# Performance work log

Hardware: AMD Instinct MI355X
Metric: run time of the kernel (lower is better)

Reference implementation:

```python
import jax, jax.numpy as jnp
import numpy as np

D_MODEL = 768
N_HEADS = 12
D_FF = 3072
EPS = 1e-5


def _dense_params(key, d_in, d_out):
    kw, kb = jax.random.split(key)
    bound = 1.0 / np.sqrt(d_in)
    W = jax.random.uniform(kw, (d_in, d_out), minval=-bound, maxval=bound, dtype=jnp.float32)
    b = jax.random.uniform(kb, (d_out,), minval=-bound, maxval=bound, dtype=jnp.float32)
    return W, b


def setup_inputs() -> dict:
    key = jax.random.key(0)
    ks = jax.random.split(key, 8)
    x = jax.random.normal(ks[0], (2, 2048, D_MODEL), dtype=jnp.float32)
    wq, bq = _dense_params(ks[1], D_MODEL, D_MODEL)
    wk, bk = _dense_params(ks[2], D_MODEL, D_MODEL)
    wv, bv = _dense_params(ks[3], D_MODEL, D_MODEL)
    wo, bo = _dense_params(ks[4], D_MODEL, D_MODEL)
    w1, b1 = _dense_params(ks[5], D_MODEL, D_FF)
    w2, b2 = _dense_params(ks[6], D_FF, D_MODEL)
    g1 = jnp.ones((D_MODEL,), jnp.float32); be1 = jnp.zeros((D_MODEL,), jnp.float32)
    g2 = jnp.ones((D_MODEL,), jnp.float32); be2 = jnp.zeros((D_MODEL,), jnp.float32)
    return {"x": x, "wq": wq, "bq": bq, "wk": wk, "bk": bk, "wv": wv, "bv": bv,
            "wo": wo, "bo": bo, "w1": w1, "b1": b1, "w2": w2, "b2": b2,
            "g1": g1, "be1": be1, "g2": g2, "be2": be2}


def _layernorm(x, g, b):
    mu = jnp.mean(x, axis=-1, keepdims=True)
    var = jnp.mean(jnp.square(x - mu), axis=-1, keepdims=True)
    return (x - mu) * jax.lax.rsqrt(var + EPS) * g + b


def reference(x, wq, bq, wk, bk, wv, bv, wo, bo, w1, b1, w2, b2, g1, be1, g2, be2):
    B, S, D = x.shape
    H, dk = N_HEADS, D // N_HEADS
    # projections -> [B, H, S, dk]
    def split_heads(t):
        return t.reshape(B, S, H, dk).transpose(0, 2, 1, 3)
    q = split_heads(x @ wq + bq)
    k = split_heads(x @ wk + bk)
    v = split_heads(x @ wv + bv)
    scores = jnp.einsum('bhqd,bhkd->bhqk', q, k) / np.sqrt(dk).astype(np.float32)
    causal = jnp.tril(jnp.ones((S, S), dtype=bool))  # True = keep
    scores = jnp.where(causal, scores, -jnp.inf)
    attn = jax.nn.softmax(scores, axis=-1)
    out = jnp.einsum('bhqk,bhkd->bhqd', attn, v)
    out = out.transpose(0, 2, 1, 3).reshape(B, S, D)
    attn_out = out @ wo + bo
    x = _layernorm(x + attn_out, g1, be1)
    ff = jax.nn.relu(x @ w1 + b1) @ w2 + b2
    x = _layernorm(x + ff, g2, be2)
    return x
```

## Files before the change

### kernel.cpp

```cpp
#include <hip/hip_runtime.h>
#include <stdint.h>

#define S_LEN 2048
#define BATCH 2
#define DM 768
#define NH 12
#define DKH 64
#define DFF 3072
#define MROWS (BATCH * S_LEN)
#define NBH (BATCH * NH)

typedef short bf16x8 __attribute__((ext_vector_type(8)));
typedef float f32x4 __attribute__((ext_vector_type(4)));
typedef float f32x16 __attribute__((ext_vector_type(16)));

__device__ __forceinline__ unsigned short f2b(float f) {
    union { float f; unsigned u; } cv; cv.f = f;
    unsigned u = cv.u;
    unsigned r = (u + 0x7FFFu + ((u >> 16) & 1u)) >> 16;
    return (unsigned short)r;
}

__device__ __forceinline__ float b2f(unsigned short u) {
    union { unsigned u; float f; } cv; cv.u = ((unsigned)u) << 16;
    return cv.f;
}

__device__ __forceinline__ void gload16(const void* g, void* l) {
    __builtin_amdgcn_global_load_lds(
        (const __attribute__((address_space(1))) unsigned int*)g,
        (__attribute__((address_space(3))) unsigned int*)l, 16, 0, 0);
}

__device__ __forceinline__ unsigned cvtpk(float lo, float hi) {
    unsigned r;
    asm("v_cvt_pk_bf16_f32 %0, %1, %2" : "=v"(r) : "v"(lo), "v"(hi));
    return r;
}
__device__ __forceinline__ void pswap(unsigned &a, unsigned &b) {
    asm("v_permlane32_swap_b32 %0, %1" : "+v"(a), "+v"(b));
}
__device__ __forceinline__ bf16x8 mkpa(unsigned w0, unsigned w1, unsigned w2, unsigned w3) {
    union { unsigned u[4]; bf16x8 h; } cv;
    cv.u[0] = w0; cv.u[1] = w1; cv.u[2] = w2; cv.u[3] = w3;
    return cv.h;
}

__global__ __launch_bounds__(256) void prep_kernel(
    const float* __restrict__ x,
    const float* __restrict__ wq, const float* __restrict__ wk,
    const float* __restrict__ wv, const float* __restrict__ wo,
    const float* __restrict__ w1, const float* __restrict__ w2,
    unsigned short* __restrict__ x16, unsigned short* __restrict__ wqkv16,
    unsigned short* __restrict__ wo16, unsigned short* __restrict__ w116,
    unsigned short* __restrict__ w216) {
    const int t = threadIdx.x;
    int bid = blockIdx.x;
    if (bid < 3072) {
        const int i = bid * 256 + t;
        float4 v = reinterpret_cast<const float4*>(x)[i];
        ushort4 o;
        o.x = f2b(v.x); o.y = f2b(v.y); o.z = f2b(v.z); o.w = f2b(v.w);
        reinterpret_cast<ushort4*>(x16)[i] = o;
        return;
    }
    bid -= 3072;
    const float* in; unsigned short* out; int R, C, bx, by;
    if (bid < 2304) {
        const int wsel = bid / 576, r = bid % 576;
        in = (wsel == 0) ? wq : (wsel == 1) ? wk : (wsel == 2) ? wv : wo;
        out = (wsel == 3) ? wo16 : wqkv16 + (size_t)wsel * DM * DM;
        R = DM; C = DM; bx = r % 24; by = r / 24;
    } else if (bid < 4608) {
        const int r = bid - 2304;
        in = w1; out = w116; R = DM; C = DFF; bx = r % 96; by = r / 96;
    } else {
        const int r = bid - 4608;
        in = w2; out = w216; R = DFF; C = DM; bx = r % 24; by = r / 24;
    }
    __shared__ float tile[32][33];
    const int c0 = bx * 32, r0 = by * 32;
    const int tx = t & 31, ty = t >> 5;
    #pragma unroll
    for (int i = ty; i < 32; i += 8)
        tile[i][tx] = in[(size_t)(r0 + i) * C + c0 + tx];
    __syncthreads();
    #pragma unroll
    for (int i = ty; i < 32; i += 8)
        out[(size_t)(c0 + i) * R + r0 + tx] = f2b(tile[tx][i]);
}

#define STG192(buf, kt)                                                                  \
    {                                                                                    \
        const char* ga = (const char*)(A + (size_t)bm * lda + koff + ((kt) << 6));       \
        const char* gb = (const char*)(Bt + (size_t)bn * ldb + koff + ((kt) << 6));      \
        char* la = (char*)Sh + (buf) * 57344 + t * 16;                                   \
        char* lb = (char*)Sh + (buf) * 57344 + 32768 + t * 16;                           \
        _Pragma("unroll")                                                                \
        for (int p = 0; p < 4; ++p)                                                      \
            gload16(ga + (size_t)(sr + p * 64) * la2 + scb_sw, la + p * 8192);           \
        _Pragma("unroll")                                                                \
        for (int p = 0; p < 3; ++p)                                                      \
            gload16(gb + (size_t)(sr + p * 64) * lb2 + scb_sw, lb + p * 8192);           \
    }

template <int EPI>
__global__ __launch_bounds__(512, 2) void gemm192(
    const unsigned short* __restrict__ A, int lda,
    const unsigned short* __restrict__ Bt, int ldb,
    const float* __restrict__ bias0, const float* __restrict__ bias1,
    const float* __restrict__ bias2,
    unsigned short* __restrict__ ob0, unsigned short* __restrict__ ob1,
    unsigned short* __restrict__ ob2, float* __restrict__ of,
    int M, int N, int Ksub, float qscale) {
    __shared__ __align__(16) unsigned short Sh[2 * 28672];
    const int t = threadIdx.x;
    const int wave = t >> 6, lane = t & 63;
    const int wr = wave >> 2, wc = wave & 3;
    const int gx = gridDim.x;
    const int nl = gx * gridDim.y;
    const int lid = blockIdx.y * gx + blockIdx.x;
    const int logical = (lid & 7) * (nl >> 3) + (lid >> 3);
    const int bn = (logical % gx) * 192, bm = (logical / gx) * 256;
    const int koff = (EPI == 3) ? blockIdx.z * Ksub : 0;
    const int lr = lane & 15;
    const int lk8 = (lane >> 4) << 3;
    const int sr = t >> 3;
    const int scb = (t & 7) * 16;
    const int scb_sw = scb ^ ((sr & 7) << 4);
    const int swr = (lr & 7) << 4;
    const size_t la2 = (size_t)lda * 2, lb2 = (size_t)ldb * 2;

    f32x4 acc[8][3];
    #pragma unroll
    for (int i = 0; i < 8; ++i)
        #pragma unroll
        for (int j = 0; j < 3; ++j) { f32x4 z = {0.f, 0.f, 0.f, 0.f}; acc[i][j] = z; }

    const int nkt = Ksub >> 6;
    STG192(0, 0)
    for (int kt = 0; kt < nkt; ++kt) {
        const int cur = kt & 1;
        if (kt + 1 < nkt) {
            STG192(cur ^ 1, kt + 1)
            asm volatile("s_waitcnt vmcnt(7)" ::: "memory");
        } else {
            asm volatile("s_waitcnt vmcnt(0)" ::: "memory");
        }
        __builtin_amdgcn_s_barrier();
        __builtin_amdgcn_sched_barrier(0);
        const char* Ab = (const char*)Sh + cur * 57344;
        const char* Bb = Ab + 32768;
        #pragma unroll
        for (int ks = 0; ks < 64; ks += 32) {
            const int cbsw = ((ks + lk8) * 2) ^ swr;
            bf16x8 af[8], bfv[3];
            #pragma unroll
            for (int i = 0; i < 8; ++i)
                af[i] = *reinterpret_cast<const bf16x8*>(Ab + (wr * 128 + i * 16 + lr) * 128 + cbsw);
            #pragma unroll
            for (int j = 0; j < 3; ++j)
                bfv[j] = *reinterpret_cast<const bf16x8*>(Bb + (wc * 48 + j * 16 + lr) * 128 + cbsw);
            __builtin_amdgcn_s_setprio(1);
            #pragma unroll
            for (int i = 0; i < 8; ++i)
                #pragma unroll
                for (int j = 0; j < 3; ++j)
                    acc[i][j] = __builtin_amdgcn_mfma_f32_16x16x32_bf16(af[i], bfv[j], acc[i][j], 0, 0, 0);
            __builtin_amdgcn_s_setprio(0);
        }
        __builtin_amdgcn_s_barrier();
    }

    const int r0 = (lane >> 4) << 2;
    if (EPI == 0) {
        #pragma unroll
        for (int i = 0; i < 8; ++i) {
            const int row_b = bm + wr * 128 + i * 16 + r0;
            #pragma unroll
            for (int j = 0; j < 3; ++j) {
                const int col = bn + wc * 48 + j * 16 + lr;
                const float bvv = bias0[col];
                #pragma unroll
                for (int r = 0; r < 4; ++r) {
                    float vv = acc[i][j][r] + bvv;
                    vv = vv > 0.f ? vv : 0.f;
                    ob0[(size_t)(row_b + r) * N + col] = f2b(vv);
                }
            }
        }
    } else if (EPI == 1) {
        const int sec = (bn >= 2 * DM) ? 2 : (bn >= DM ? 1 : 0);
        const int nb = bn - sec * DM;
        const float* bias = (sec == 0) ? bias0 : (sec == 1 ? bias1 : bias2);
        #pragma unroll
        for (int i = 0; i < 8; ++i) {
            const int row_b = bm + wr * 128 + i * 16 + r0;
            const int b = row_b >> 11, s = row_b & 2047;
            #pragma unroll
            for (int j = 0; j < 3; ++j) {
                const int c768 = nb + wc * 48 + j * 16 + lr;
                const int h = c768 >> 6, d = c768 & 63;
                const float bvv = bias[c768];
                if (sec == 2) {
                    ushort4 w;
                    w.x = f2b(acc[i][j][0] + bvv);
                    w.y = f2b(acc[i][j][1] + bvv);
                    w.z = f2b(acc[i][j][2] + bvv);
                    w.w = f2b(acc[i][j][3] + bvv);
                    *reinterpret_cast<ushort4*>(
                        ob2 + (((size_t)(b * NH + h) * DKH) + d) * S_LEN + s) = w;
                } else {
                    const float sc = (sec == 0) ? qscale : 1.f;
                    unsigned short* dst = (sec == 0) ? ob0 : ob1;
                    #pragma unroll
                    for (int r = 0; r < 4; ++r)
                        dst[(((size_t)(b * NH + h) * S_LEN) + s + r) * DKH + d] =
                            f2b((acc[i][j][r] + bvv) * sc);
                }
            }
        }
    } else {
        unsigned short* op = ob0 + (size_t)blockIdx.z * M * N;
        #pragma unroll
        for (int i = 0; i < 8; ++i) {
            const int row_b = bm + wr * 128 + i * 16 + r0;
            #pragma unroll
            for (int j = 0; j < 3; ++j) {
                const int col = bn + wc * 48 + j * 16 + lr;
                #pragma unroll
                for (int r = 0; r < 4; ++r)
                    op[(size_t)(row_b + r) * N + col] = f2b(acc[i][j][r]);
            }
        }
    }
}

#define STAGEKV(buf, kt)                                                              \
    {                                                                                 \
        const char* kg = kbyte + (((size_t)(kt)) << 13);                              \
        const char* vg = vbyte + (((size_t)(kt)) << 7);                               \
        char* lk = (char*)&KV[buf][0][0] + lane * 16;                                 \
        char* lv = (char*)&KV[buf][1][0] + lane * 16;                                 \
        _Pragma("unroll")                                                             \
        for (int i = 0; i < 8; ++i)                                                   \
            gload16(kg + (i * 8 + sub) * 128 + ccs, lk + i * 1024);                   \
        _Pragma("unroll")                                                             \
        for (int i = 0; i < 8; ++i)                                                   \
            gload16(vg + (size_t)(i * 8 + sub) * (S_LEN * 2) + ccs, lv + i * 1024);   \
    }

__global__ __launch_bounds__(64) void attn_mfma_kernel(
    const unsigned short* __restrict__ q16,
    const unsigned short* __restrict__ k16,
    const unsigned short* __restrict__ vt16,
    unsigned short* __restrict__ ctx16) {
    __shared__ __align__(16) char KV[2][2][8192];
    const int lane = threadIdx.x & 63;
    const int bh = blockIdx.x;
    const int qb = (gridDim.y - 1) - blockIdx.y;
    const int b = bh / NH, h = bh % NH;
    const size_t hbase = (size_t)bh * S_LEN * DKH;
    const int x = lane & 31;
    const int hi = lane >> 5;
    const int k8 = hi << 3;
    const int sW = qb << 5;
    const int qg = sW + x;
    const int sub = lane >> 3;
    const int ccs = ((lane & 7) * 16) ^ (sub << 4);
    const int swz = (x & 7) << 4;

    bf16x8 qa[4];
    #pragma unroll
    for (int c = 0; c < 4; ++c)
        qa[c] = *reinterpret_cast<const bf16x8*>(
            q16 + hbase + (size_t)(sW + x) * DKH + c * 16 + k8);

    float mst = -3e38f, lst = 0.f;
    f32x16 acc0, acc1;
    #pragma unroll
    for (int r = 0; r < 16; ++r) { acc0[r] = 0.f; acc1[r] = 0.f; }

    const char* kbyte = (const char*)(k16 + hbase);
    const char* vbyte = (const char*)(vt16 + hbase);
    const int nt = (sW >> 6) + 1;

    STAGEKV(0, 0)
    for (int kt = 0; kt < nt; ++kt) {
        const int cur = kt & 1;
        asm volatile("s_waitcnt vmcnt(0)" ::: "memory");
        if (kt + 1 < nt) STAGEKV(cur ^ 1, kt + 1)
        const char* Kb = (const char*)&KV[cur][0][0];
        const char* Vb = (const char*)&KV[cur][1][0];
        const int k0 = kt << 6;

        bf16x8 kaf[2][4];
        #pragma unroll
        for (int kh = 0; kh < 2; ++kh)
            #pragma unroll
            for (int c = 0; c < 4; ++c)
                kaf[kh][c] = *reinterpret_cast<const bf16x8*>(
                    Kb + (kh * 32 + x) * 128 + ((c * 32 + hi * 16) ^ swz));

        f32x16 sc0, sc1;
        #pragma unroll
        for (int r = 0; r < 16; ++r) { sc0[r] = 0.f; sc1[r] = 0.f; }
        __builtin_amdgcn_s_setprio(1);
        #pragma unroll
        for (int c = 0; c < 4; ++c) {
            sc0 = __builtin_amdgcn_mfma_f32_32x32x16_bf16(kaf[0][c], qa[c], sc0, 0, 0, 0);
            sc1 = __builtin_amdgcn_mfma_f32_32x32x16_bf16(kaf[1][c], qa[c], sc1, 0, 0, 0);
        }
        __builtin_amdgcn_s_setprio(0);

        if (kt == nt - 1) {
            #pragma unroll
            for (int r = 0; r < 16; ++r) {
                const int cr = (r & 3) + (hi << 2) + ((r >> 2) << 3);
                if (k0 + cr > qg) sc0[r] = -3e38f;
                if (k0 + 32 + cr > qg) sc1[r] = -3e38f;
            }
        }

        float tm = fmaxf(sc0[0], sc0[1]);
        #pragma unroll
        for (int r = 2; r < 16; ++r) tm = fmaxf(tm, sc0[r]);
        #pragma unroll
        for (int r = 0; r < 16; ++r) tm = fmaxf(tm, sc1[r]);
        tm = fmaxf(tm, __shfl_xor(tm, 32));

        if (!__all(tm <= mst + 8.f)) {
            const float mn = fmaxf(mst, tm);
            const float corr = exp2f(mst - mn);
            mst = mn;
            lst *= corr;
            float cw[16];
            #pragma unroll
            for (int r = 0; r < 16; ++r)
                cw[r] = __shfl(corr, (r & 3) + (hi << 2) + ((r >> 2) << 3));
            #pragma unroll
            for (int r = 0; r < 16; ++r) { acc0[r] *= cw[r]; acc1[r] *= cw[r]; }
        }

        float ts = 0.f;
        #pragma unroll
        for (int r = 0; r < 16; ++r) {
            sc0[r] = exp2f(sc0[r] - mst); ts += sc0[r];
            sc1[r] = exp2f(sc1[r] - mst); ts += sc1[r];
        }
        ts += __shfl_xor(ts, 32);
        lst += ts;

        unsigned a0 = cvtpk(sc0[0], sc0[1]),   b0 = cvtpk(sc0[4], sc0[5]);   pswap(a0, b0);
        unsigned a1 = cvtpk(sc0[2], sc0[3]),   b1 = cvtpk(sc0[6], sc0[7]);   pswap(a1, b1);
        unsigned a2 = cvtpk(sc0[8], sc0[9]),   b2 = cvtpk(sc0[12], sc0[13]); pswap(a2, b2);
        unsigned a3 = cvtpk(sc0[10], sc0[11]), b3 = cvtpk(sc0[14], sc0[15]); pswap(a3, b3);
        bf16x8 pa00 = mkpa(a0, a1, b0, b1);
        bf16x8 pa01 = mkpa(a2, a3, b2, b3);
        unsigned c0 = cvtpk(sc1[0], sc1[1]),   d0 = cvtpk(sc1[4], sc1[5]);   pswap(c0, d0);
        unsigned c1 = cvtpk(sc1[2], sc1[3]),   d1 = cvtpk(sc1[6], sc1[7]);   pswap(c1, d1);
        unsigned c2 = cvtpk(sc1[8], sc1[9]),   d2 = cvtpk(sc1[12], sc1[13]); pswap(c2, d2);
        unsigned c3 = cvtpk(sc1[10], sc1[11]), d3 = cvtpk(sc1[14], sc1[15]); pswap(c3, d3);
        bf16x8 pa10 = mkpa(c0, c1, d0, d1);
        bf16x8 pa11 = mkpa(c2, c3, d2, d3);

        bf16x8 vaf[2][4];
        #pragma unroll
        for (int dt = 0; dt < 2; ++dt)
            #pragma unroll
            for (int s = 0; s < 4; ++s)
                vaf[dt][s] = *reinterpret_cast<const bf16x8*>(
                    Vb + (dt * 32 + x) * 128 + ((s * 32 + hi * 16) ^ swz));

        __builtin_amdgcn_s_setprio(1);
        acc0 = __builtin_amdgcn_mfma_f32_32x32x16_bf16(pa00, vaf[0][0], acc0, 0, 0, 0);
        acc1 = __builtin_amdgcn_mfma_f32_32x32x16_bf16(pa00, vaf[1][0], acc1, 0, 0, 0);
        acc0 = __builtin_amdgcn_mfma_f32_32x32x16_bf16(pa01, vaf[0][1], acc0, 0, 0, 0);
        acc1 = __builtin_amdgcn_mfma_f32_32x32x16_bf16(pa01, vaf[1][1], acc1, 0, 0, 0);
        acc0 = __builtin_amdgcn_mfma_f32_32x32x16_bf16(pa10, vaf[0][2], acc0, 0, 0, 0);
        acc1 = __builtin_amdgcn_mfma_f32_32x32x16_bf16(pa10, vaf[1][2], acc1, 0, 0, 0);
        acc0 = __builtin_amdgcn_mfma_f32_32x32x16_bf16(pa11, vaf[0][3], acc0, 0, 0, 0);
        acc1 = __builtin_amdgcn_mfma_f32_32x32x16_bf16(pa11, vaf[1][3], acc1, 0, 0, 0);
        __builtin_amdgcn_s_setprio(0);
    }

    const float li = 1.f / lst;
    float lw[16];
    #pragma unroll
    for (int r = 0; r < 16; ++r)
        lw[r] = __shfl(li, (r & 3) + (hi << 2) + ((r >> 2) << 3));
    #pragma unroll
    for (int r = 0; r < 16; ++r) {
        const int q = sW + (r & 3) + (hi << 2) + ((r >> 2) << 3);
        const size_t rowb = ((size_t)b * S_LEN + q) * DM + h * DKH;
        ctx16[rowb + x] = f2b(acc0[r] * lw[r]);
        ctx16[rowb + 32 + x] = f2b(acc1[r] * lw[r]);
    }
}

template <int EB16OUT, int RES16>
__global__ __launch_bounds__(192) void ln_merge_kernel(
    const unsigned short* __restrict__ part, size_t pstride, int ns,
    const void* __restrict__ res, const float* __restrict__ bias,
    const float* __restrict__ gam, const float* __restrict__ bet,
    float* __restrict__ outf, unsigned short* __restrict__ outb) {
    __shared__ float red[8];
    const int row = blockIdx.x, t = threadIdx.x;
    const int wave = t >> 6, lane = t & 63;
    const size_t base = (size_t)row * DM;
    float4 v;
    if (RES16) {
        const ushort4 rv = reinterpret_cast<const ushort4*>((const unsigned short*)res + base)[t];
        v.x = b2f(rv.x); v.y = b2f(rv.y); v.z = b2f(rv.z); v.w = b2f(rv.w);
    } else {
        v = reinterpret_cast<const float4*>((const float*)res + base)[t];
    }
    const float4 bv = reinterpret_cast<const float4*>(bias)[t];
    v.x += bv.x; v.y += bv.y; v.z += bv.z; v.w += bv.w;
    for (int z = 0; z < ns; ++z) {
        const ushort4 p = reinterpret_cast<const ushort4*>(part + (size_t)z * pstride + base)[t];
        v.x += b2f(p.x); v.y += b2f(p.y); v.z += b2f(p.z); v.w += b2f(p.w);
    }
    float s = v.x + v.y + v.z + v.w;
    float sq = v.x * v.x + v.y * v.y + v.z * v.z + v.w * v.w;
    #pragma unroll
    for (int off = 32; off > 0; off >>= 1) { s += __shfl_xor(s, off); sq += __shfl_xor(sq, off); }
    if (lane == 0) { red[wave] = s; red[wave + 4] = sq; }
    __syncthreads();
    s = red[0] + red[1] + red[2];
    sq = red[4] + red[5] + red[6];
    const float mu = s * (1.f / DM);
    const float var = sq * (1.f / DM) - mu * mu;
    const float rs = rsqrtf(var + 1e-5f);
    const float4 g = reinterpret_cast<const float4*>(gam)[t];
    const float4 be = reinterpret_cast<const float4*>(bet)[t];
    float4 o;
    o.x = (v.x - mu) * rs * g.x + be.x;
    o.y = (v.y - mu) * rs * g.y + be.y;
    o.z = (v.z - mu) * rs * g.z + be.z;
    o.w = (v.w - mu) * rs * g.w + be.w;
    if (EB16OUT) {
        ushort4 ob;
        ob.x = f2b(o.x); ob.y = f2b(o.y); ob.z = f2b(o.z); ob.w = f2b(o.w);
        reinterpret_cast<ushort4*>(outb + base)[t] = ob;
    } else {
        reinterpret_cast<float4*>(outf + base)[t] = o;
    }
}

extern "C" void kernel_launch(void* const* d_in, const int* in_sizes, int n_in,
                              void* d_out, int out_size, void* d_ws, size_t ws_size,
                              hipStream_t stream) {
    const float* x   = (const float*)d_in[0];
    const float* wq  = (const float*)d_in[1];
    const float* bq  = (const float*)d_in[2];
    const float* wk  = (const float*)d_in[3];
    const float* bk  = (const float*)d_in[4];
    const float* wv  = (const float*)d_in[5];
    const float* bv  = (const float*)d_in[6];
    const float* wo  = (const float*)d_in[7];
    const float* bo  = (const float*)d_in[8];
    const float* w1  = (const float*)d_in[9];
    const float* b1  = (const float*)d_in[10];
    const float* w2  = (const float*)d_in[11];
    const float* b2  = (const float*)d_in[12];
    const float* g1  = (const float*)d_in[13];
    const float* be1 = (const float*)d_in[14];
    const float* g2  = (const float*)d_in[15];
    const float* be2 = (const float*)d_in[16];

    char* wp = (char*)d_ws;
    auto alloc = [&](size_t bytes) -> void* {
        void* r = (void*)wp;
        wp += (bytes + 255) & ~(size_t)255;
        return r;
    };
    const int M = MROWS;
    unsigned short* wqkv16 = (unsigned short*)alloc((size_t)3 * DM * DM * 2);
    unsigned short* wo16 = (unsigned short*)alloc((size_t)DM * DM * 2);
    unsigned short* w116 = (unsigned short*)alloc((size_t)DM * DFF * 2);
    unsigned short* w216 = (unsigned short*)alloc((size_t)DM * DFF * 2);
    unsigned short* ctx16 = (unsigned short*)alloc((size_t)M * DM * 2);
    unsigned short* x16  = (unsigned short*)alloc((size_t)M * DM * 2);
    unsigned short* q16  = (unsigned short*)alloc((size_t)M * DM * 2);
    unsigned short* k16  = (unsigned short*)alloc((size_t)M * DM * 2);
    unsigned short* vt16 = (unsigned short*)alloc((size_t)M * DM * 2);
    unsigned short* ff116 = x16;
    unsigned short* x116  = ctx16;

    const size_t perb = (size_t)M * DM * 2;
    size_t used = (size_t)(wp - (char*)d_ws);
    int NS = 1;
    if (used + 4 * perb + 1024 <= ws_size) NS = 4;
    else if (used + 2 * perb + 1024 <= ws_size) NS = 2;
    unsigned short* part = (unsigned short*)alloc((size_t)NS * perb);
    const int NSW = (NS >= 2) ? 2 : 1;

    prep_kernel<<<9984, 256, 0, stream>>>(x, wq, wk, wv, wo, w1, w2,
                                          x16, wqkv16, wo16, w116, w216);

    const float QSCALE = 0.125f * 1.44269504088896f;
    gemm192<1><<<dim3(3 * DM / 192, M / 256), 512, 0, stream>>>(
        x16, DM, wqkv16, DM, bq, bk, bv, q16, k16, vt16, nullptr, M, 3 * DM, DM, QSCALE);

    attn_mfma_kernel<<<dim3(NBH, S_LEN / 32), 64, 0, stream>>>(q16, k16, vt16, ctx16);

    gemm192<3><<<dim3(DM / 192, M / 256, NSW), 512, 0, stream>>>(
        ctx16, DM, wo16, DM, nullptr, nullptr, nullptr, part, nullptr, nullptr, nullptr,
        M, DM, DM / NSW, 1.f);
    ln_merge_kernel<1, 0><<<M, 192, 0, stream>>>(part, (size_t)M * DM, NSW, x, bo, g1, be1,
                                                 nullptr, x116);

    gemm192<0><<<dim3(DFF / 192, M / 256), 512, 0, stream>>>(
        x116, DM, w116, DM, b1, nullptr, nullptr, ff116, nullptr, nullptr, nullptr, M, DFF, DM, 1.f);

    gemm192<3><<<dim3(DM / 192, M / 256, NS), 512, 0, stream>>>(
        ff116, DFF, w216, DFF, nullptr, nullptr, nullptr, part, nullptr, nullptr, nullptr,
        M, DM, DFF / NS, 1.f);
    ln_merge_kernel<0, 1><<<M, 192, 0, stream>>>(part, (size_t)M * DM, NS, x116, b2, g2, be2,
                                                 (float*)d_out, nullptr);
}
```

Measured before the change: 172.9 us.

## Split GEMM K-tile prefetch into staggered sub-loads interleaved with MFMA phases

The 192-wide bf16 GEMM main loop now issues its global-to-LDS loads in pieces spread across four MFMA phases, instead of staging the whole next tile at once. Row-quarters of A and the B tile are prefetched up to two K-steps ahead, wherever the LDS regions they overwrite have already been consumed. Each half K-step is split into two half-row MFMA groups separated by barriers, and vmcnt waits are set to match the new load order. The goal is to spread memory traffic evenly and hide load latency behind compute. The cost is extra workgroup barriers and a more fragile buffer-reuse ordering.

Result: no change. 173.3 us (+0.2%).

```diff
diff --git a/kernel.cpp b/kernel.cpp
--- a/kernel.cpp
+++ b/kernel.cpp
@@ -90,18 +90,17 @@
         out[(size_t)(c0 + i) * R + r0 + tx] = f2b(tile[tx][i]);
 }
 
-#define STG192(buf, kt)                                                                  \
-    {                                                                                    \
-        const char* ga = (const char*)(A + (size_t)bm * lda + koff + ((kt) << 6));       \
-        const char* gb = (const char*)(Bt + (size_t)bn * ldb + koff + ((kt) << 6));      \
-        char* la = (char*)Sh + (buf) * 57344 + t * 16;                                   \
-        char* lb = (char*)Sh + (buf) * 57344 + 32768 + t * 16;                           \
-        _Pragma("unroll")                                                                \
-        for (int p = 0; p < 4; ++p)                                                      \
-            gload16(ga + (size_t)(sr + p * 64) * la2 + scb_sw, la + p * 8192);           \
-        _Pragma("unroll")                                                                \
-        for (int p = 0; p < 3; ++p)                                                      \
-            gload16(gb + (size_t)(sr + p * 64) * lb2 + scb_sw, lb + p * 8192);           \
+#define SA192(buf, kt, p)                                                                 \
+    gload16((const char*)(A + (size_t)bm * lda + koff + ((kt) << 6)) +                    \
+                (size_t)(sr + (p) * 64) * la2 + scb_sw,                                   \
+            (char*)Sh + (buf) * 57344 + (p) * 8192 + t * 16);
+#define SB192(buf, kt)                                                                    \
+    {                                                                                     \
+        const char* gb_ = (const char*)(Bt + (size_t)bn * ldb + koff + ((kt) << 6));      \
+        char* lb_ = (char*)Sh + (buf) * 57344 + 32768 + t * 16;                           \
+        _Pragma("unroll")                                                                 \
+        for (int p = 0; p < 3; ++p)                                                       \
+            gload16(gb_ + (size_t)(sr + p * 64) * lb2 + scb_sw, lb_ + p * 8192);          \
     }
 
 template <int EPI>
@@ -138,37 +137,79 @@
         for (int j = 0; j < 3; ++j) { f32x4 z = {0.f, 0.f, 0.f, 0.f}; acc[i][j] = z; }
 
     const int nkt = Ksub >> 6;
-    STG192(0, 0)
+    SA192(0, 0, 0) SA192(0, 0, 1) SA192(0, 0, 2) SA192(0, 0, 3) SB192(0, 0)
+    if (nkt > 1) { SA192(1, 1, 0) SA192(1, 1, 2) SB192(1, 1) }
+
     for (int kt = 0; kt < nkt; ++kt) {
         const int cur = kt & 1;
-        if (kt + 1 < nkt) {
-            STG192(cur ^ 1, kt + 1)
-            asm volatile("s_waitcnt vmcnt(7)" ::: "memory");
-        } else {
-            asm volatile("s_waitcnt vmcnt(0)" ::: "memory");
-        }
+        if (kt + 1 < nkt) asm volatile("s_waitcnt vmcnt(5)" ::: "memory");
+        else              asm volatile("s_waitcnt vmcnt(0)" ::: "memory");
         __builtin_amdgcn_s_barrier();
         __builtin_amdgcn_sched_barrier(0);
         const char* Ab = (const char*)Sh + cur * 57344;
         const char* Bb = Ab + 32768;
-        #pragma unroll
-        for (int ks = 0; ks < 64; ks += 32) {
-            const int cbsw = ((ks + lk8) * 2) ^ swr;
-            bf16x8 af[8], bfv[3];
-            #pragma unroll
-            for (int i = 0; i < 8; ++i)
-                af[i] = *reinterpret_cast<const bf16x8*>(Ab + (wr * 128 + i * 16 + lr) * 128 + cbsw);
+        const int cb0 = ((0 + lk8) * 2) ^ swr;
+        const int cb1 = ((32 + lk8) * 2) ^ swr;
+        bf16x8 afh[4], bfv[3];
+
+        if (kt + 1 < nkt) { SA192(cur ^ 1, kt + 1, 1) SA192(cur ^ 1, kt + 1, 3) }
+        #pragma unroll
+        for (int i = 0; i < 4; ++i)
+            afh[i] = *reinterpret_cast<const bf16x8*>(Ab + (wr * 128 + i * 16 + lr) * 128 + cb0);
+        #pragma unroll
+        for (int j = 0; j < 3; ++j)
+            bfv[j] = *reinterpret_cast<const bf16x8*>(Bb + (wc * 48 + j * 16 + lr) * 128 + cb0);
+        __builtin_amdgcn_s_barrier();
+        __builtin_amdgcn_s_setprio(1);
+        #pragma unroll
+        for (int i = 0; i < 4; ++i)
             #pragma unroll
             for (int j = 0; j < 3; ++j)
-                bfv[j] = *reinterpret_cast<const bf16x8*>(Bb + (wc * 48 + j * 16 + lr) * 128 + cbsw);
-            __builtin_amdgcn_s_setprio(1);
-            #pragma unroll
-            for (int i = 0; i < 8; ++i)
-                #pragma unroll
-                for (int j = 0; j < 3; ++j)
-                    acc[i][j] = __builtin_amdgcn_mfma_f32_16x16x32_bf16(af[i], bfv[j], acc[i][j], 0, 0, 0);
-            __builtin_amdgcn_s_setprio(0);
-        }
+                acc[i][j] = __builtin_amdgcn_mfma_f32_16x16x32_bf16(afh[i], bfv[j], acc[i][j], 0, 0, 0);
+        __builtin_amdgcn_s_setprio(0);
+        __builtin_amdgcn_s_barrier();
+
+        #pragma unroll
+        for (int i = 0; i < 4; ++i)
+            afh[i] = *reinterpret_cast<const bf16x8*>(Ab + (wr * 128 + (i + 4) * 16 + lr) * 128 + cb0);
+        __builtin_amdgcn_s_barrier();
+        __builtin_amdgcn_s_setprio(1);
+        #pragma unroll
+        for (int i = 0; i < 4; ++i)
+            #pragma unroll
+            for (int j = 0; j < 3; ++j)
+                acc[i + 4][j] = __builtin_amdgcn_mfma_f32_16x16x32_bf16(afh[i], bfv[j], acc[i + 4][j], 0, 0, 0);
+        __builtin_amdgcn_s_setprio(0);
+        __builtin_amdgcn_s_barrier();
+
+        #pragma unroll
+        for (int i = 0; i < 4; ++i)
+            afh[i] = *reinterpret_cast<const bf16x8*>(Ab + (wr * 128 + i * 16 + lr) * 128 + cb1);
+        #pragma unroll
+        for (int j = 0; j < 3; ++j)
+            bfv[j] = *reinterpret_cast<const bf16x8*>(Bb + (wc * 48 + j * 16 + lr) * 128 + cb1);
+        __builtin_amdgcn_s_barrier();
+        __builtin_amdgcn_s_setprio(1);
+        #pragma unroll
+        for (int i = 0; i < 4; ++i)
+            #pragma unroll
+            for (int j = 0; j < 3; ++j)
+                acc[i][j] = __builtin_amdgcn_mfma_f32_16x16x32_bf16(afh[i], bfv[j], acc[i][j], 0, 0, 0);
+        __builtin_amdgcn_s_setprio(0);
+        __builtin_amdgcn_s_barrier();
+
+        if (kt + 2 < nkt) { SA192(cur, kt + 2, 0) SA192(cur, kt + 2, 2) SB192(cur, kt + 2) }
+        #pragma unroll
+        for (int i = 0; i < 4; ++i)
+            afh[i] = *reinterpret_cast<const bf16x8*>(Ab + (wr * 128 + (i + 4) * 16 + lr) * 128 + cb1);
+        __builtin_amdgcn_s_barrier();
+        __builtin_amdgcn_s_setprio(1);
+        #pragma unroll
+        for (int i = 0; i < 4; ++i)
+            #pragma unroll
+            for (int j = 0; j < 3; ++j)
+                acc[i + 4][j] = __builtin_amdgcn_mfma_f32_16x16x32_bf16(afh[i], bfv[j], acc[i + 4][j], 0, 0, 0);
+        __builtin_amdgcn_s_setprio(0);
         __builtin_amdgcn_s_barrier();
     }
 
```

## Software-pipeline attention with triple-buffered KV and QK of next tile issued early

Applied to the files above, without the earlier changes.

The attention kernel moves from double to triple buffering of the K/V tiles in LDS. It computes the QK^T MFMA for tile kt+1 before the softmax and PV work of tile kt, and prefetches tile kt+2. It uses a partial vmcnt wait so that only the K half of the next tile must have landed. The aim is to overlap the matrix work with softmax and the global-to-LDS loads. In exchange it uses more LDS and more score registers, and the last iteration no longer waits explicitly for its V loads, which could be a race.

Result: slower. 180.4 us (+4.3%).

```diff
diff --git a/kernel.cpp b/kernel.cpp
--- a/kernel.cpp
+++ b/kernel.cpp
@@ -236,12 +236,13 @@
     }
 }
 
-#define STAGEKV(buf, kt)                                                              \
+#define STAGEKV(kt)                                                                   \
     {                                                                                 \
+        char* bb = (char*)KV + ((kt) % 3) * 16384;                                    \
         const char* kg = kbyte + (((size_t)(kt)) << 13);                              \
         const char* vg = vbyte + (((size_t)(kt)) << 7);                               \
-        char* lk = (char*)&KV[buf][0][0] + lane * 16;                                 \
-        char* lv = (char*)&KV[buf][1][0] + lane * 16;                                 \
+        char* lk = bb + lane * 16;                                                    \
+        char* lv = bb + 8192 + lane * 16;                                             \
         _Pragma("unroll")                                                             \
         for (int i = 0; i < 8; ++i)                                                   \
             gload16(kg + (i * 8 + sub) * 128 + ccs, lk + i * 1024);                   \
@@ -250,12 +251,31 @@
             gload16(vg + (size_t)(i * 8 + sub) * (S_LEN * 2) + ccs, lv + i * 1024);   \
     }
 
+#define QKTILE(kt, d0, d1)                                                            \
+    {                                                                                 \
+        const char* Kb_ = (const char*)KV + ((kt) % 3) * 16384;                       \
+        bf16x8 kaf[2][4];                                                             \
+        _Pragma("unroll")                                                             \
+        for (int kh = 0; kh < 2; ++kh)                                                \
+            _Pragma("unroll")                                                         \
+            for (int c = 0; c < 4; ++c)                                               \
+                kaf[kh][c] = *reinterpret_cast<const bf16x8*>(                        \
+                    Kb_ + (kh * 32 + x) * 128 + ((c * 32 + hi * 16) ^ swz));          \
+        __builtin_amdgcn_s_setprio(1);                                                \
+        _Pragma("unroll")                                                             \
+        for (int c = 0; c < 4; ++c) {                                                 \
+            d0 = __builtin_amdgcn_mfma_f32_32x32x16_bf16(kaf[0][c], qa[c], d0, 0, 0, 0); \
+            d1 = __builtin_amdgcn_mfma_f32_32x32x16_bf16(kaf[1][c], qa[c], d1, 0, 0, 0); \
+        }                                                                             \
+        __builtin_amdgcn_s_setprio(0);                                                \
+    }
+
 __global__ __launch_bounds__(64) void attn_mfma_kernel(
     const unsigned short* __restrict__ q16,
     const unsigned short* __restrict__ k16,
     const unsigned short* __restrict__ vt16,
     unsigned short* __restrict__ ctx16) {
-    __shared__ __align__(16) char KV[2][2][8192];
+    __shared__ __align__(16) char KV[3 * 16384];
     const int lane = threadIdx.x & 63;
     const int bh = blockIdx.x;
     const int qb = (gridDim.y - 1) - blockIdx.y;
@@ -285,33 +305,25 @@
     const char* vbyte = (const char*)(vt16 + hbase);
     const int nt = (sW >> 6) + 1;
 
-    STAGEKV(0, 0)
+    STAGEKV(0)
+    asm volatile("s_waitcnt vmcnt(0)" ::: "memory");
+    if (nt > 1) STAGEKV(1)
+    f32x16 sc0, sc1;
+    #pragma unroll
+    for (int r = 0; r < 16; ++r) { sc0[r] = 0.f; sc1[r] = 0.f; }
+    QKTILE(0, sc0, sc1)
+
     for (int kt = 0; kt < nt; ++kt) {
-        const int cur = kt & 1;
-        asm volatile("s_waitcnt vmcnt(0)" ::: "memory");
-        if (kt + 1 < nt) STAGEKV(cur ^ 1, kt + 1)
-        const char* Kb = (const char*)&KV[cur][0][0];
-        const char* Vb = (const char*)&KV[cur][1][0];
         const int k0 = kt << 6;
 
-        bf16x8 kaf[2][4];
-        #pragma unroll
-        for (int kh = 0; kh < 2; ++kh)
-            #pragma unroll
-            for (int c = 0; c < 4; ++c)
-                kaf[kh][c] = *reinterpret_cast<const bf16x8*>(
-                    Kb + (kh * 32 + x) * 128 + ((c * 32 + hi * 16) ^ swz));
-
-        f32x16 sc0, sc1;
-        #pragma unroll
-        for (int r = 0; r < 16; ++r) { sc0[r] = 0.f; sc1[r] = 0.f; }
-        __builtin_amdgcn_s_setprio(1);
-        #pragma unroll
-        for (int c = 0; c < 4; ++c) {
-            sc0 = __builtin_amdgcn_mfma_f32_32x32x16_bf16(kaf[0][c], qa[c], sc0, 0, 0, 0);
-            sc1 = __builtin_amdgcn_mfma_f32_32x32x16_bf16(kaf[1][c], qa[c], sc1, 0, 0, 0);
-        }
-        __builtin_amdgcn_s_setprio(0);
+        f32x16 sn0, sn1;
+        #pragma unroll
+        for (int r = 0; r < 16; ++r) { sn0[r] = 0.f; sn1[r] = 0.f; }
+        if (kt + 1 < nt) {
+            asm volatile("s_waitcnt vmcnt(8)" ::: "memory");
+            if (kt + 2 < nt) STAGEKV(kt + 2)
+            QKTILE(kt + 1, sn0, sn1)
+        }
 
         if (kt == nt - 1) {
             #pragma unroll
@@ -364,6 +376,7 @@
         bf16x8 pa10 = mkpa(c0, c1, d0, d1);
         bf16x8 pa11 = mkpa(c2, c3, d2, d3);
 
+        const char* Vb = (const char*)KV + (kt % 3) * 16384 + 8192;
         bf16x8 vaf[2][4];
         #pragma unroll
         for (int dt = 0; dt < 2; ++dt)
@@ -382,6 +395,8 @@
         acc0 = __builtin_amdgcn_mfma_f32_32x32x16_bf16(pa11, vaf[0][3], acc0, 0, 0, 0);
         acc1 = __builtin_amdgcn_mfma_f32_32x32x16_bf16(pa11, vaf[1][3], acc1, 0, 0, 0);
         __builtin_amdgcn_s_setprio(0);
+
+        sc0 = sn0; sc1 = sn1;
     }
 
     const float li = 1.f / lst;
```
